# Optimization experiments

Hardware: AMD Instinct MI355X
Metric: run time of the kernel (lower is better)

The kernel has to match this reference:

```python
import jax, jax.numpy as jnp
import numpy as np
from jax import lax

B, S, D_IN = 4, 4096, 1024
D_FAST, D_SLOW = 512, 512
Z_BIAS_FAST, Z_BIAS_SLOW = 2.0, -2.0


def _binop(q_i, q_j):
    a_i, b_i = q_i
    a_j, b_j = q_j
    return (a_i * a_j, a_j * b_i + b_j)


def parallel_scan(a, b):
    # h_t = a_t * h_{t-1} + b_t along seq axis (axis=1)
    _, h = lax.associative_scan(_binop, (a, b), axis=1)
    return h


def setup_inputs() -> dict:
    key = jax.random.key(0)
    ks = jax.random.split(key, 6)
    scale = 0.02
    x = jax.random.normal(ks[0], (B, S, D_IN), dtype=jnp.float32)
    W_zf = jax.random.normal(ks[1], (D_IN, D_FAST), dtype=jnp.float32) * scale
    b_zf = jnp.full((D_FAST,), Z_BIAS_FAST, dtype=jnp.float32)
    W_hf = jax.random.normal(ks[2], (D_IN, D_FAST), dtype=jnp.float32) * scale
    b_hf = jnp.zeros((D_FAST,), dtype=jnp.float32)
    W_zs = jax.random.normal(ks[3], (D_IN, D_SLOW), dtype=jnp.float32) * scale
    b_zs = jnp.full((D_SLOW,), Z_BIAS_SLOW, dtype=jnp.float32)
    W_hs = jax.random.normal(ks[4], (D_IN, D_SLOW), dtype=jnp.float32) * scale
    b_hs = jnp.zeros((D_SLOW,), dtype=jnp.float32)
    W_g = jax.random.normal(ks[5], (D_FAST + D_SLOW, D_FAST + D_SLOW), dtype=jnp.float32) * scale
    b_g = jnp.zeros((D_FAST + D_SLOW,), dtype=jnp.float32)
    return {"x": x, "W_zf": W_zf, "b_zf": b_zf, "W_hf": W_hf, "b_hf": b_hf,
            "W_zs": W_zs, "b_zs": b_zs, "W_hs": W_hs, "b_hs": b_hs,
            "W_g": W_g, "b_g": b_g}


def reference(x, W_zf, b_zf, W_hf, b_hf, W_zs, b_zs, W_hs, b_hs, W_g, b_g):
    # Fast compartment (coupling='output' => slow branch sees raw x)
    z_fast = jax.nn.sigmoid(jnp.einsum('bsd,df->bsf', x, W_zf) + b_zf)
    h_tilde_fast = jnp.einsum('bsd,df->bsf', x, W_hf) + b_hf
    h_fast = parallel_scan(1.0 - z_fast, z_fast * h_tilde_fast)

    # Slow compartment
    z_slow = jax.nn.sigmoid(jnp.einsum('bsd,df->bsf', x, W_zs) + b_zs)
    h_tilde_slow = jnp.einsum('bsd,df->bsf', x, W_hs) + b_hs
    h_slow = parallel_scan(1.0 - z_slow, z_slow * h_tilde_slow)

    h_combined = jnp.concatenate([h_fast, h_slow], axis=-1)  # (B, S, D_FAST+D_SLOW)
    gate = jax.nn.sigmoid(jnp.einsum('bsc,cd->bsd', h_combined, W_g) + b_g)
    return gate * h_combined
```

## Files before the change

kernel.cpp:

```cpp
#include <hip/hip_runtime.h>

#define BB 4
#define SS 4096
#define DIN 1024
#define DH 1024
#define PN 2048
#define MM (BB*SS)
#define NC 64
#define CL 64

typedef unsigned short ushort_t;
typedef __attribute__((ext_vector_type(8))) short bf16x8;
typedef __attribute__((ext_vector_type(8))) unsigned short u16x8;
typedef __attribute__((ext_vector_type(4))) float f32x4;
typedef __attribute__((ext_vector_type(4))) unsigned short u16x4;

__device__ inline float bf2f(ushort_t u) {
    union { float f; unsigned int i; } v; v.i = ((unsigned int)u) << 16; return v.f;
}
__device__ inline ushort_t f2bf(float f) {
    union { float f; unsigned int i; } v; v.f = f;
    unsigned int r = v.i + 0x7fffu + ((v.i >> 16) & 1u);
    return (ushort_t)(r >> 16);
}
__device__ inline float sigmoidf_(float x) { return 1.0f / (1.0f + __expf(-x)); }

__device__ inline void load_lds16(const void* g, void* l) {
    __builtin_amdgcn_global_load_lds(
        (const __attribute__((address_space(1))) void*)g,
        (__attribute__((address_space(3))) void*)l, 16, 0, 0);
}

__global__ void zero_out_kernel(float* out, int n) {
    int i = blockIdx.x * 256 + threadIdx.x;
    if (i < n) out[i] = 0.0f;
}

#define PREP_NBLK 17160
__global__ __launch_bounds__(256) void prep_kernel(
    const float* __restrict__ x,
    const float* __restrict__ Wzf, const float* __restrict__ Wzs,
    const float* __restrict__ Whf, const float* __restrict__ Whs,
    const float* __restrict__ Wg,
    const float* __restrict__ bzf, const float* __restrict__ bzs,
    const float* __restrict__ bhf, const float* __restrict__ bhs,
    ushort_t* __restrict__ WcatT, ushort_t* __restrict__ WgT,
    ushort_t* __restrict__ Xb, float* __restrict__ bcat)
{
    __shared__ ushort_t tile[64][65];
    const int bx = blockIdx.x, tid = threadIdx.x;

    if (bx < 768) {
        const float* src; ushort_t* dst; int srcN, t;
        if (bx < 512) {
            int wi = bx >> 7; t = bx & 127; srcN = 512;
            const float* S[4] = {Wzf, Wzs, Whf, Whs};
            src = S[wi];
            dst = WcatT + (size_t)(wi * 512) * DIN;
        } else {
            t = bx - 512; srcN = 1024; src = Wg; dst = WgT;
        }
        const int k0 = (t & 15) * 64, n0 = (t >> 4) * 64;
        const int tx = tid & 63, ty = tid >> 6;
        #pragma unroll
        for (int i = ty; i < 64; i += 4)
            tile[i][tx] = f2bf(src[(size_t)(k0 + i) * srcN + n0 + tx]);
        __syncthreads();
        #pragma unroll
        for (int i = ty; i < 64; i += 4)
            dst[(size_t)(n0 + i) * DIN + k0 + tx] = tile[tx][i];
    } else if (bx < 17152) {
        size_t i = ((size_t)(bx - 768) * 256 + tid) * 4;
        float4 v = *(const float4*)(x + i);
        u16x4 o;
        o.x = f2bf(v.x); o.y = f2bf(v.y); o.z = f2bf(v.z); o.w = f2bf(v.w);
        *(u16x4*)(Xb + i) = o;
    } else {
        int i = (bx - 17152) * 256 + tid;
        float v = (i < 512) ? bzf[i] : (i < 1024) ? bzs[i - 512]
                : (i < 1536) ? bhf[i - 1024] : bhs[i - 1536];
        bcat[i] = v;
    }
}

#define NB1 (PN/128)
__global__ __launch_bounds__(256) void gemm1_mfma(
    const ushort_t* __restrict__ A, const ushort_t* __restrict__ Bt,
    const float* __restrict__ bias,
    ushort_t* __restrict__ Zarr, ushort_t* __restrict__ Harr)
{
    __shared__ alignas(16) unsigned char smem[34816];
    ushort_t* As  = (ushort_t*)smem;
    ushort_t* Bs  = (ushort_t*)(smem + 16384);
    ushort_t* R16 = (ushort_t*)smem;

    const int tid  = threadIdx.x;
    const int lane = tid & 63;
    const int wave = tid >> 6;
    const int wm   = wave & 1;
    const int wn   = wave >> 1;
    const int lrow = lane & 15;
    const int kgrp = lane >> 4;

    const int id  = blockIdx.x;
    const int xcd = id & 7;
    const int s   = id >> 3;
    const int mBase = (xcd + 8 * (s / NB1)) * 128;
    const int nBase = (s % NB1) * 128;

    f32x4 acc[4][4] = {};
    const ushort_t* Ablk = A  + (size_t)mBase * DIN;
    const ushort_t* Bblk = Bt + (size_t)nBase * DIN;

    for (int k0 = 0; k0 < DIN; k0 += 64) {
        #pragma unroll
        for (int i = 0; i < 4; i++) {
            int idx = i * 256 + tid;
            int r   = idx >> 3;
            int cc  = ((idx & 7) ^ (r & 7)) * 8;
            load_lds16(Ablk + (size_t)r * DIN + k0 + cc, &As[idx * 8]);
            load_lds16(Bblk + (size_t)r * DIN + k0 + cc, &Bs[idx * 8]);
        }
        __syncthreads();
        #pragma unroll
        for (int kk = 0; kk < 64; kk += 32) {
            const int c0 = (kk >> 3) + kgrp;
            bf16x8 af[4], bfr[4];
            #pragma unroll
            for (int mt = 0; mt < 4; mt++) {
                int r = wm * 64 + mt * 16 + lrow;
                af[mt] = *(const bf16x8*)&As[r * 64 + (c0 ^ (r & 7)) * 8];
            }
            #pragma unroll
            for (int nt = 0; nt < 4; nt++) {
                int r = wn * 64 + nt * 16 + lrow;
                bfr[nt] = *(const bf16x8*)&Bs[r * 64 + (c0 ^ (r & 7)) * 8];
            }
            #pragma unroll
            for (int mt = 0; mt < 4; mt++)
                #pragma unroll
                for (int nt = 0; nt < 4; nt++)
                    acc[mt][nt] = __builtin_amdgcn_mfma_f32_16x16x32_bf16(
                        af[mt], bfr[nt], acc[mt][nt], 0, 0, 0);
        }
        __syncthreads();
    }

    const bool isz = (nBase < DH);
    ushort_t* Dst  = isz ? Zarr : Harr;
    const int dcb  = nBase - (isz ? 0 : DH);
    const int rquad = (lane >> 4) * 4;

    #pragma unroll
    for (int nt = 0; nt < 4; nt++) {
        int colrel = wn * 64 + nt * 16 + lrow;
        float bv = bias[nBase + colrel];
        #pragma unroll
        for (int mt = 0; mt < 4; mt++) {
            int rowrel = wm * 64 + mt * 16 + rquad;
            #pragma unroll
            for (int r = 0; r < 4; r++) {
                float v = acc[mt][nt][r] + bv;
                if (isz) v = sigmoidf_(v);
                R16[(rowrel + r) * 136 + colrel] = f2bf(v);
            }
        }
    }
    __syncthreads();
    #pragma unroll
    for (int it = 0; it < 8; it++) {
        int cid = it * 256 + tid;
        int rr  = cid >> 4, cc = (cid & 15) * 8;
        u16x8 v = *(const u16x8*)&R16[rr * 136 + cc];
        *(u16x8*)&Dst[(size_t)(mBase + rr) * DH + dcb + cc] = v;
    }
}

#define NB2 (DH/128)
__global__ __launch_bounds__(256) void gemm2_mfma(
    const ushort_t* __restrict__ A, const ushort_t* __restrict__ Bt,
    const float* __restrict__ bg, float* __restrict__ Out)
{
    __shared__ alignas(16) unsigned char smem[34816];
    ushort_t* As  = (ushort_t*)smem;
    ushort_t* Bs  = (ushort_t*)(smem + 16384);
    float*    R32 = (float*)smem;

    const int tid  = threadIdx.x;
    const int lane = tid & 63;
    const int wave = tid >> 6;
    const int wm   = wave & 1;
    const int wn   = wave >> 1;
    const int lrow = lane & 15;
    const int kgrp = lane >> 4;
    const int rquad = (lane >> 4) * 4;

    const int id  = blockIdx.x;
    const int xcd = id & 7;
    const int s   = id >> 3;
    const int mBase = (xcd + 8 * (s / NB2)) * 128;
    const int nBase = (s % NB2) * 128;

    f32x4 acc[4][4] = {};
    ushort_t hcap[4][4][4];
    const int kcap = nBase + wn * 64;

    const ushort_t* Ablk = A  + (size_t)mBase * DH;
    const ushort_t* Bblk = Bt + (size_t)nBase * DIN;

    for (int k0 = 0; k0 < DIN; k0 += 64) {
        #pragma unroll
        for (int i = 0; i < 4; i++) {
            int idx = i * 256 + tid;
            int r   = idx >> 3;
            int cc  = ((idx & 7) ^ (r & 7)) * 8;
            load_lds16(Ablk + (size_t)r * DH  + k0 + cc, &As[idx * 8]);
            load_lds16(Bblk + (size_t)r * DIN + k0 + cc, &Bs[idx * 8]);
        }
        __syncthreads();

        if (k0 == kcap) {
            #pragma unroll
            for (int mt = 0; mt < 4; mt++)
                #pragma unroll
                for (int r = 0; r < 4; r++) {
                    int rrr = wm * 64 + mt * 16 + rquad + r;
                    int sw  = rrr & 7;
                    #pragma unroll
                    for (int nt = 0; nt < 4; nt++) {
                        int ck = nt * 16 + lrow;
                        hcap[mt][nt][r] = As[rrr * 64 + (((ck >> 3) ^ sw) * 8) + (ck & 7)];
                    }
                }
        }

        #pragma unroll
        for (int kk = 0; kk < 64; kk += 32) {
            const int c0 = (kk >> 3) + kgrp;
            bf16x8 af[4], bfr[4];
            #pragma unroll
            for (int mt = 0; mt < 4; mt++) {
                int r = wm * 64 + mt * 16 + lrow;
                af[mt] = *(const bf16x8*)&As[r * 64 + (c0 ^ (r & 7)) * 8];
            }
            #pragma unroll
            for (int nt = 0; nt < 4; nt++) {
                int r = wn * 64 + nt * 16 + lrow;
                bfr[nt] = *(const bf16x8*)&Bs[r * 64 + (c0 ^ (r & 7)) * 8];
            }
            #pragma unroll
            for (int mt = 0; mt < 4; mt++)
                #pragma unroll
                for (int nt = 0; nt < 4; nt++)
                    acc[mt][nt] = __builtin_amdgcn_mfma_f32_16x16x32_bf16(
                        af[mt], bfr[nt], acc[mt][nt], 0, 0, 0);
        }
        __syncthreads();
    }

    #pragma unroll
    for (int h = 0; h < 2; h++) {
        if (wm == h) {
            #pragma unroll
            for (int nt = 0; nt < 4; nt++) {
                int colrel = wn * 64 + nt * 16 + lrow;
                float bv = bg[nBase + colrel];
                #pragma unroll
                for (int mt = 0; mt < 4; mt++) {
                    int rloc = mt * 16 + rquad;
                    #pragma unroll
                    for (int r = 0; r < 4; r++) {
                        float g  = sigmoidf_(acc[mt][nt][r] + bv);
                        float hv = bf2f(hcap[mt][nt][r]);
                        R32[(rloc + r) * 132 + colrel] = g * hv;
                    }
                }
            }
        }
        __syncthreads();
        #pragma unroll
        for (int it = 0; it < 8; it++) {
            int cid = it * 256 + tid;
            int rr  = cid >> 5, cc4 = (cid & 31) * 4;
            float4 v = *(const float4*)&R32[rr * 132 + cc4];
            *(float4*)&Out[(size_t)(mBase + h * 64 + rr) * DH + nBase + cc4] = v;
        }
        __syncthreads();
    }
}

__global__ __launch_bounds__(256) void scan_chunk_agg(
    const ushort_t* __restrict__ Zarr, const ushort_t* __restrict__ Harr,
    float* __restrict__ Agg, float* __restrict__ Bagg)
{
    const int c4    = threadIdx.x * 4;
    const int chunk = blockIdx.x;
    const int b     = blockIdx.y;
    const size_t s0 = ((size_t)b * SS + (size_t)chunk * CL) * DH + c4;
    const ushort_t* Zp = Zarr + s0;
    const ushort_t* Hp = Harr + s0;

    float A0 = 1.0f, A1 = 1.0f, A2 = 1.0f, A3 = 1.0f;
    float B0 = 0.0f, B1 = 0.0f, B2 = 0.0f, B3 = 0.0f;
    #pragma unroll 8
    for (int t = 0; t < CL; t++) {
        u16x4 zv = *(const u16x4*)(Zp + (size_t)t * DH);
        u16x4 hv = *(const u16x4*)(Hp + (size_t)t * DH);
        float z0 = bf2f(zv.x), z1 = bf2f(zv.y), z2 = bf2f(zv.z), z3 = bf2f(zv.w);
        float h0 = bf2f(hv.x), h1 = bf2f(hv.y), h2 = bf2f(hv.z), h3 = bf2f(hv.w);
        A0 *= 1.0f - z0;  B0 = (1.0f - z0) * B0 + z0 * h0;
        A1 *= 1.0f - z1;  B1 = (1.0f - z1) * B1 + z1 * h1;
        A2 *= 1.0f - z2;  B2 = (1.0f - z2) * B2 + z2 * h2;
        A3 *= 1.0f - z3;  B3 = (1.0f - z3) * B3 + z3 * h3;
    }
    const size_t idx = ((size_t)(b * NC + chunk)) * DH + c4;
    *(float4*)(Agg  + idx) = make_float4(A0, A1, A2, A3);
    *(float4*)(Bagg + idx) = make_float4(B0, B1, B2, B3);
}

__global__ void scan_carry(const float* __restrict__ Agg, const float* __restrict__ Bagg,
                           float* __restrict__ Hinit)
{
    const int i = blockIdx.x * 256 + threadIdx.x;
    const int b = i >> 10, c = i & 1023;
    float h = 0.0f;
    for (int j = 0; j < NC; j++) {
        const size_t idx = ((size_t)(b * NC + j)) * DH + c;
        Hinit[idx] = h;
        h = Agg[idx] * h + Bagg[idx];
    }
}

__global__ __launch_bounds__(256) void scan_apply(
    const ushort_t* __restrict__ Zarr, ushort_t* Harr, const float* __restrict__ Hinit)
{
    const int c4    = threadIdx.x * 4;
    const int chunk = blockIdx.x;
    const int b     = blockIdx.y;
    const size_t s0 = ((size_t)b * SS + (size_t)chunk * CL) * DH + c4;
    const ushort_t* Zp = Zarr + s0;
    ushort_t*       Hp = Harr + s0;

    float4 hi = *(const float4*)(Hinit + ((size_t)(b * NC + chunk)) * DH + c4);
    float h0 = hi.x, h1 = hi.y, h2 = hi.z, h3 = hi.w;
    #pragma unroll 8
    for (int t = 0; t < CL; t++) {
        u16x4 zv = *(const u16x4*)(Zp + (size_t)t * DH);
        u16x4 hv = *(const u16x4*)(Hp + (size_t)t * DH);
        float z0 = bf2f(zv.x), z1 = bf2f(zv.y), z2 = bf2f(zv.z), z3 = bf2f(zv.w);
        float t0 = bf2f(hv.x), t1 = bf2f(hv.y), t2 = bf2f(hv.z), t3 = bf2f(hv.w);
        h0 = (1.0f - z0) * h0 + z0 * t0;
        h1 = (1.0f - z1) * h1 + z1 * t1;
        h2 = (1.0f - z2) * h2 + z2 * t2;
        h3 = (1.0f - z3) * h3 + z3 * t3;
        u16x4 o;
        o.x = f2bf(h0); o.y = f2bf(h1); o.z = f2bf(h2); o.w = f2bf(h3);
        *(u16x4*)(Hp + (size_t)t * DH) = o;
    }
}

extern "C" void kernel_launch(void* const* d_in, const int* in_sizes, int n_in,
                              void* d_out, int out_size, void* d_ws, size_t ws_size,
                              hipStream_t stream)
{
    const float* x   = (const float*)d_in[0];
    const float* Wzf = (const float*)d_in[1];
    const float* bzf = (const float*)d_in[2];
    const float* Whf = (const float*)d_in[3];
    const float* bhf = (const float*)d_in[4];
    const float* Wzs = (const float*)d_in[5];
    const float* bzs = (const float*)d_in[6];
    const float* Whs = (const float*)d_in[7];
    const float* bhs = (const float*)d_in[8];
    const float* Wg  = (const float*)d_in[9];
    const float* bg  = (const float*)d_in[10];

    const size_t NEED = (size_t)42 << 20;
    if (ws_size < NEED) {
        zero_out_kernel<<<(MM * DH + 255) / 256, 256, 0, stream>>>((float*)d_out, MM * DH);
        return;
    }

    char* ws = (char*)d_ws;
    ushort_t* WcatT = (ushort_t*)(ws);
    ushort_t* WgT   = (ushort_t*)(ws + ((size_t)4 << 20));
    float*    bcat  = (float*)   (ws + ((size_t)6 << 20));
    float*    Agg   = (float*)   (ws + ((size_t)6 << 20) + (64 << 10));
    float*    Bagg  = (float*)   (ws + ((size_t)7 << 20) + (64 << 10));
    float*    Hinit = (float*)   (ws + ((size_t)8 << 20) + (64 << 10));
    ushort_t* Harr  = (ushort_t*)(ws + ((size_t)10 << 20));

    ushort_t* Xb   = (ushort_t*)d_out;
    ushort_t* Zarr = Xb + (size_t)MM * DH;

    dim3 blk(256);

    prep_kernel<<<PREP_NBLK, blk, 0, stream>>>(
        x, Wzf, Wzs, Whf, Whs, Wg, bzf, bzs, bhf, bhs, WcatT, WgT, Xb, bcat);

    gemm1_mfma<<<(MM / 128) * NB1, blk, 0, stream>>>(Xb, WcatT, bcat, Zarr, Harr);

    scan_chunk_agg<<<dim3(NC, BB), blk, 0, stream>>>(Zarr, Harr, Agg, Bagg);
    scan_carry<<<16, 256, 0, stream>>>(Agg, Bagg, Hinit);
    scan_apply<<<dim3(NC, BB), blk, 0, stream>>>(Zarr, Harr, Hinit);

    gemm2_mfma<<<(MM / 128) * NB2, blk, 0, stream>>>(Harr, WgT, bg, (float*)d_out);
}
```

Baseline: 377.1 us.

## Drop scan_carry kernel, write GEMM epilogues directly, reload H tile in gemm2

Removes the separate scan_carry launch: each scan_apply block now recomputes its chunk carry by serially combining the preceding chunk aggregates. gemm1 no longer stages its output tile through LDS and writes bf16 values straight to global memory as scattered 2-byte stores. gemm2 drops the in-loop capture of the H values and instead reloads the H tile from global into LDS after the main loop, then writes fp32 outputs with per-element stores. The aim is to save a launch and LDS round-trips, at the cost of uncoalesced global stores and redundant carry work.

New measurement: 340.6 us. 9.7% less time.

```diff
diff --git a/kernel.cpp b/kernel.cpp
--- a/kernel.cpp
+++ b/kernel.cpp
@@ -89,10 +89,8 @@
     const float* __restrict__ bias,
     ushort_t* __restrict__ Zarr, ushort_t* __restrict__ Harr)
 {
-    __shared__ alignas(16) unsigned char smem[34816];
-    ushort_t* As  = (ushort_t*)smem;
-    ushort_t* Bs  = (ushort_t*)(smem + 16384);
-    ushort_t* R16 = (ushort_t*)smem;
+    __shared__ alignas(16) ushort_t As[128 * 64];
+    __shared__ alignas(16) ushort_t Bs[128 * 64];
 
     const int tid  = threadIdx.x;
     const int lane = tid & 63;
@@ -148,43 +146,38 @@
 
     const bool isz = (nBase < DH);
     ushort_t* Dst  = isz ? Zarr : Harr;
-    const int dcb  = nBase - (isz ? 0 : DH);
+    const int csub = isz ? 0 : DH;
+    const int row0  = mBase + wm * 64;
+    const int col0  = nBase + wn * 64;
     const int rquad = (lane >> 4) * 4;
 
     #pragma unroll
     for (int nt = 0; nt < 4; nt++) {
-        int colrel = wn * 64 + nt * 16 + lrow;
-        float bv = bias[nBase + colrel];
+        int col  = col0 + nt * 16 + lrow;
+        float bv = bias[col];
+        int dcol = col - csub;
         #pragma unroll
         for (int mt = 0; mt < 4; mt++) {
-            int rowrel = wm * 64 + mt * 16 + rquad;
+            int row = row0 + mt * 16 + rquad;
+            ushort_t* p = Dst + (size_t)row * DH + dcol;
             #pragma unroll
             for (int r = 0; r < 4; r++) {
                 float v = acc[mt][nt][r] + bv;
                 if (isz) v = sigmoidf_(v);
-                R16[(rowrel + r) * 136 + colrel] = f2bf(v);
-            }
-        }
-    }
-    __syncthreads();
-    #pragma unroll
-    for (int it = 0; it < 8; it++) {
-        int cid = it * 256 + tid;
-        int rr  = cid >> 4, cc = (cid & 15) * 8;
-        u16x8 v = *(const u16x8*)&R16[rr * 136 + cc];
-        *(u16x8*)&Dst[(size_t)(mBase + rr) * DH + dcb + cc] = v;
+                p[(size_t)r * DH] = f2bf(v);
+            }
+        }
     }
 }
 
 #define NB2 (DH/128)
 __global__ __launch_bounds__(256) void gemm2_mfma(
     const ushort_t* __restrict__ A, const ushort_t* __restrict__ Bt,
-    const float* __restrict__ bg, float* __restrict__ Out)
-{
-    __shared__ alignas(16) unsigned char smem[34816];
-    ushort_t* As  = (ushort_t*)smem;
-    ushort_t* Bs  = (ushort_t*)(smem + 16384);
-    float*    R32 = (float*)smem;
+    const float* __restrict__ bg, const ushort_t* __restrict__ Hbf,
+    float* __restrict__ Out)
+{
+    __shared__ alignas(16) ushort_t As[128 * 64];
+    __shared__ alignas(16) ushort_t Bs[128 * 64];
 
     const int tid  = threadIdx.x;
     const int lane = tid & 63;
@@ -193,7 +186,6 @@
     const int wn   = wave >> 1;
     const int lrow = lane & 15;
     const int kgrp = lane >> 4;
-    const int rquad = (lane >> 4) * 4;
 
     const int id  = blockIdx.x;
     const int xcd = id & 7;
@@ -202,9 +194,6 @@
     const int nBase = (s % NB2) * 128;
 
     f32x4 acc[4][4] = {};
-    ushort_t hcap[4][4][4];
-    const int kcap = nBase + wn * 64;
-
     const ushort_t* Ablk = A  + (size_t)mBase * DH;
     const ushort_t* Bblk = Bt + (size_t)nBase * DIN;
 
@@ -218,22 +207,6 @@
             load_lds16(Bblk + (size_t)r * DIN + k0 + cc, &Bs[idx * 8]);
         }
         __syncthreads();
-
-        if (k0 == kcap) {
-            #pragma unroll
-            for (int mt = 0; mt < 4; mt++)
-                #pragma unroll
-                for (int r = 0; r < 4; r++) {
-                    int rrr = wm * 64 + mt * 16 + rquad + r;
-                    int sw  = rrr & 7;
-                    #pragma unroll
-                    for (int nt = 0; nt < 4; nt++) {
-                        int ck = nt * 16 + lrow;
-                        hcap[mt][nt][r] = As[rrr * 64 + (((ck >> 3) ^ sw) * 8) + (ck & 7)];
-                    }
-                }
-        }
-
         #pragma unroll
         for (int kk = 0; kk < 64; kk += 32) {
             const int c0 = (kk >> 3) + kgrp;
@@ -258,34 +231,39 @@
         __syncthreads();
     }
 
+    ushort_t* Hs = As;
     #pragma unroll
-    for (int h = 0; h < 2; h++) {
-        if (wm == h) {
-            #pragma unroll
-            for (int nt = 0; nt < 4; nt++) {
-                int colrel = wn * 64 + nt * 16 + lrow;
-                float bv = bg[nBase + colrel];
-                #pragma unroll
-                for (int mt = 0; mt < 4; mt++) {
-                    int rloc = mt * 16 + rquad;
-                    #pragma unroll
-                    for (int r = 0; r < 4; r++) {
-                        float g  = sigmoidf_(acc[mt][nt][r] + bv);
-                        float hv = bf2f(hcap[mt][nt][r]);
-                        R32[(rloc + r) * 132 + colrel] = g * hv;
-                    }
-                }
-            }
-        }
-        __syncthreads();
-        #pragma unroll
-        for (int it = 0; it < 8; it++) {
-            int cid = it * 256 + tid;
-            int rr  = cid >> 5, cc4 = (cid & 31) * 4;
-            float4 v = *(const float4*)&R32[rr * 132 + cc4];
-            *(float4*)&Out[(size_t)(mBase + h * 64 + rr) * DH + nBase + cc4] = v;
-        }
-        __syncthreads();
+    for (int it = 0; it < 8; it++) {
+        int cid = it * 256 + tid;
+        int rr  = cid >> 4;
+        int c   = cid & 15;
+        int p   = c ^ (rr & 7);
+        u16x8 v = *(const u16x8*)&Hbf[(size_t)(mBase + rr) * DH + nBase + c * 8];
+        *(u16x8*)&Hs[rr * 128 + p * 8] = v;
+    }
+    __syncthreads();
+
+    const int row0  = mBase + wm * 64;
+    const int col0  = nBase + wn * 64;
+    const int rquad = (lane >> 4) * 4;
+
+    #pragma unroll
+    for (int nt = 0; nt < 4; nt++) {
+        int colrel = wn * 64 + nt * 16 + lrow;
+        int col    = nBase + colrel;
+        float bv   = bg[col];
+        int ck = colrel >> 3, c7 = colrel & 7;
+        #pragma unroll
+        for (int mt = 0; mt < 4; mt++) {
+            int rowrel0 = wm * 64 + mt * 16 + rquad;
+            #pragma unroll
+            for (int r = 0; r < 4; r++) {
+                int rr = rowrel0 + r;
+                float h = bf2f(Hs[rr * 128 + ((ck ^ (rr & 7)) * 8) + c7]);
+                float g = sigmoidf_(acc[mt][nt][r] + bv);
+                Out[(size_t)(row0 + mt * 16 + rquad + r) * DH + col] = g * h;
+            }
+        }
     }
 }
 
@@ -318,31 +296,28 @@
     *(float4*)(Bagg + idx) = make_float4(B0, B1, B2, B3);
 }
 
-__global__ void scan_carry(const float* __restrict__ Agg, const float* __restrict__ Bagg,
-                           float* __restrict__ Hinit)
-{
-    const int i = blockIdx.x * 256 + threadIdx.x;
-    const int b = i >> 10, c = i & 1023;
-    float h = 0.0f;
-    for (int j = 0; j < NC; j++) {
-        const size_t idx = ((size_t)(b * NC + j)) * DH + c;
-        Hinit[idx] = h;
-        h = Agg[idx] * h + Bagg[idx];
-    }
-}
-
 __global__ __launch_bounds__(256) void scan_apply(
-    const ushort_t* __restrict__ Zarr, ushort_t* Harr, const float* __restrict__ Hinit)
+    const ushort_t* __restrict__ Zarr, ushort_t* Harr,
+    const float* __restrict__ Agg, const float* __restrict__ Bagg)
 {
     const int c4    = threadIdx.x * 4;
     const int chunk = blockIdx.x;
     const int b     = blockIdx.y;
+
+    float h0 = 0.0f, h1 = 0.0f, h2 = 0.0f, h3 = 0.0f;
+    for (int jj = 0; jj < chunk; jj++) {
+        const size_t idx = ((size_t)(b * NC + jj)) * DH + c4;
+        float4 Av = *(const float4*)(Agg  + idx);
+        float4 Bv = *(const float4*)(Bagg + idx);
+        h0 = Av.x * h0 + Bv.x;
+        h1 = Av.y * h1 + Bv.y;
+        h2 = Av.z * h2 + Bv.z;
+        h3 = Av.w * h3 + Bv.w;
+    }
+
     const size_t s0 = ((size_t)b * SS + (size_t)chunk * CL) * DH + c4;
     const ushort_t* Zp = Zarr + s0;
     ushort_t*       Hp = Harr + s0;
-
-    float4 hi = *(const float4*)(Hinit + ((size_t)(b * NC + chunk)) * DH + c4);
-    float h0 = hi.x, h1 = hi.y, h2 = hi.z, h3 = hi.w;
     #pragma unroll 8
     for (int t = 0; t < CL; t++) {
         u16x4 zv = *(const u16x4*)(Zp + (size_t)t * DH);
@@ -387,7 +362,6 @@
     float*    bcat  = (float*)   (ws + ((size_t)6 << 20));
     float*    Agg   = (float*)   (ws + ((size_t)6 << 20) + (64 << 10));
     float*    Bagg  = (float*)   (ws + ((size_t)7 << 20) + (64 << 10));
-    float*    Hinit = (float*)   (ws + ((size_t)8 << 20) + (64 << 10));
     ushort_t* Harr  = (ushort_t*)(ws + ((size_t)10 << 20));
 
     ushort_t* Xb   = (ushort_t*)d_out;
@@ -401,8 +375,7 @@
     gemm1_mfma<<<(MM / 128) * NB1, blk, 0, stream>>>(Xb, WcatT, bcat, Zarr, Harr);
 
     scan_chunk_agg<<<dim3(NC, BB), blk, 0, stream>>>(Zarr, Harr, Agg, Bagg);
-    scan_carry<<<16, 256, 0, stream>>>(Agg, Bagg, Hinit);
-    scan_apply<<<dim3(NC, BB), blk, 0, stream>>>(Zarr, Harr, Hinit);
-
-    gemm2_mfma<<<(MM / 128) * NB2, blk, 0, stream>>>(Harr, WgT, bg, (float*)d_out);
-}
+    scan_apply<<<dim3(NC, BB), blk, 0, stream>>>(Zarr, Harr, Agg, Bagg);
+
+    gemm2_mfma<<<(MM / 128) * NB2, blk, 0, stream>>>(Harr, WgT, bg, Harr, (float*)d_out);
+}
```
